# Kernel tuning notes

Hardware: AMD Instinct MI355X
Metric: run time of the kernel (lower is better)

The kernel has to match this reference:

```python
import jax, jax.numpy as jnp
import numpy as np

K = 31   # avg_pool2d kernel_size
PAD = 15 # avg_pool2d padding (count_include_pad=True -> divide by K*K always)


def box_mean(x):
    # x: (N, C, H, W). Zero-padded 31x31 box filter, stride 1, same output size.
    s = jax.lax.reduce_window(
        x, 0.0, jax.lax.add,
        window_dimensions=(1, 1, K, K),
        window_strides=(1, 1, 1, 1),
        padding=((0, 0), (0, 0), (PAD, PAD), (PAD, PAD)))
    return s / (K * K)


def setup_inputs() -> dict:
    key = jax.random.key(0)
    k1, k2 = jax.random.split(key)
    N, C, H, W = 16, 2, 512, 512
    pred = jax.random.normal(k1, (N, C, H, W), dtype=jnp.float32)
    target = jax.random.randint(k2, (N, H, W), 0, C)  # class labels in [0, C)
    return {"pred": pred, "target": target}


def reference(pred, target):
    LOSS_WEIGHT = 1.0
    N, C, H, W = pred.shape
    # _expand_onehot_labels: clamp to [0, C], one-hot C+1, drop last, NHWC->NCHW
    t = jnp.clip(target, 0, C)
    mask = jnp.transpose(jax.nn.one_hot(t, C + 1, dtype=pred.dtype)[..., :C],
                         (0, 3, 1, 2))  # (N, C, H, W), float
    # ignore_index=255 > C so the channel filter keeps all channels (no-op)

    weit = 1.0 + 5.0 * jnp.abs(box_mean(mask) - mask)

    # F.binary_cross_entropy_with_logits(pred, mask, reduce='none'):
    # legacy `reduce='none'` is truthy -> reduction='mean' in torch, so wbce is
    # the GLOBAL mean of elementwise BCE; the subsequent weighted normalization
    # (weit*wbce).sum/weit.sum is then an identity broadcast. Replicated faithfully.
    bce = jnp.maximum(pred, 0.0) - pred * mask + jnp.log1p(jnp.exp(-jnp.abs(pred)))
    wbce = jnp.mean(bce)  # scalar

    p = jax.nn.sigmoid(pred)
    inter = jnp.sum(p * mask * weit, axis=(2, 3))          # (N, C)
    union = jnp.sum((p + mask) * weit, axis=(2, 3))        # (N, C)
    wiou = 1.0 - (inter + 1.0) / (union - inter + 1.0)     # (N, C)

    return LOSS_WEIGHT * jnp.mean(wbce + wiou)
```

## Files before the change

kernel.cpp:

```cpp
#include <hip/hip_runtime.h>
#include <stdint.h>

#define N_IMG 16
#define H_DIM 512
#define W_DIM 512
#define PADR 15
#define BAND 8
#define HALO (BAND + 2 * PADR)
#define WPR 18
#define NBANDS (H_DIM / BAND)
#define WROW (W_DIM / 32)


__global__ __launch_bounds__(512) void bitmap_kernel(const int* __restrict__ target,
                                                     uint32_t* __restrict__ bm) {
    const int tid = threadIdx.x;
    const size_t idx = (size_t)blockIdx.x * 512 + tid;
    const int t = target[idx];
    const unsigned long long bal = __ballot(t == 1);
    if ((tid & 31) == 0)
        bm[idx >> 5] = (tid & 32) ? (uint32_t)(bal >> 32) : (uint32_t)bal;
}

__global__ __launch_bounds__(512, 8) void mega_kernel(const uint32_t* __restrict__ bm,
                                                      const float* __restrict__ pred,
                                                      float* __restrict__ part) {
    __shared__ uint32_t B[HALO][WPR];
    const int tid = threadIdx.x;
    const int band = blockIdx.x;
    const int n = blockIdx.y;
    const int r0 = band * BAND;
    const int col = tid;

    const uint32_t* __restrict__ bmn = bm + (size_t)n * H_DIM * WROW;
    const int hr0 = tid >> 4, wi = tid & 15;
    const int ra = r0 - PADR + hr0;
    uint32_t w0 = 0, w1 = 0;
    if (ra >= 0 && ra < H_DIM) w0 = bmn[ra * WROW + wi];
    const int hr1 = hr0 + 32;
    const int rb = r0 - PADR + hr1;
    if (tid < 96 && rb >= 0 && rb < H_DIM) w1 = bmn[rb * WROW + wi];

    const size_t img = (size_t)n * H_DIM * W_DIM;
    const float* __restrict__ p0 = pred + img * 2 + (size_t)r0 * W_DIM + col;
    const float* __restrict__ p1 = p0 + (size_t)H_DIM * W_DIM;
    float x0[BAND], x1[BAND];
#pragma unroll
    for (int rr = 0; rr < BAND; ++rr) {
        x0[rr] = p0[rr * W_DIM];
        x1[rr] = p1[rr * W_DIM];
    }

    if (tid < 2 * HALO) B[tid >> 1][(tid & 1) ? (WPR - 1) : 0] = 0u;
    B[hr0][1 + wi] = w0;
    if (tid < 96) B[hr1][1 + wi] = w1;
    __syncthreads();

    const int b = col + (32 - PADR);
    const int q = b >> 5, s = b & 31;
    auto wpop = [&](int i) -> uint32_t {
        const uint32_t lo = B[i][q];
        const uint32_t hi = B[i][q + 1];
        const uint32_t val =
            (uint32_t)((((uint64_t)hi << 32) | lo) >> s) & 0x7FFFFFFFu;
        return val;
    };

    uint32_t run = 0, mbits = 0;
#pragma unroll
    for (int i = 0; i < 31; ++i) {
        const uint32_t val = wpop(i);
        run += (uint32_t)__popc(val);
        if (i >= PADR && i < PADR + BAND)
            mbits |= ((val >> PADR) & 1u) << (i - PADR);
    }

    const int cntw = min(col + PADR, W_DIM - 1) - max(col - PADR, 0) + 1;
    const float inv961 = 1.0f / 961.0f;
    float bce = 0.f, in0 = 0.f, in1 = 0.f, un0 = 0.f, un1 = 0.f;

#pragma unroll
    for (int rr = 0; rr < BAND; ++rr) {
        const int r = r0 + rr;
        const int cnth = min(r + PADR, H_DIM - 1) - max(r - PADR, 0) + 1;
        const float cnt = (float)(cnth * cntw);
        const float m1 = (float)((mbits >> rr) & 1u);
        const float m0 = 1.0f - m1;
        const float V = (float)run;
        const float box1 = V * inv961;
        const float box0 = (cnt - V) * inv961;
        const float w1f = 1.0f + 5.0f * fabsf(box1 - m1);
        const float w0f = 1.0f + 5.0f * fabsf(box0 - m0);
        {
            const float x = x0[rr];
            const float t = __expf(-fabsf(x));
            const float inv = 1.0f / (1.0f + t);
            const float p = (x >= 0.f) ? inv : t * inv;
            bce += fmaxf(x, 0.f) - x * m0 + __logf(1.0f + t);
            in0 += p * m0 * w0f;
            un0 += (p + m0) * w0f;
        }
        {
            const float x = x1[rr];
            const float t = __expf(-fabsf(x));
            const float inv = 1.0f / (1.0f + t);
            const float p = (x >= 0.f) ? inv : t * inv;
            bce += fmaxf(x, 0.f) - x * m1 + __logf(1.0f + t);
            in1 += p * m1 * w1f;
            un1 += (p + m1) * w1f;
        }
        if (rr < BAND - 1)
            run += (uint32_t)__popc(wpop(rr + 31)) - (uint32_t)__popc(wpop(rr));
    }

    __shared__ float red[8 * 5];
    const int lane = tid & 63, wv = tid >> 6;
    float v[5] = {bce, in0, in1, un0, un1};
#pragma unroll
    for (int k = 0; k < 5; ++k)
#pragma unroll
        for (int off = 32; off > 0; off >>= 1)
            v[k] += __shfl_down(v[k], off);
    if (lane == 0)
#pragma unroll
        for (int k = 0; k < 5; ++k) red[wv * 5 + k] = v[k];
    __syncthreads();
    if (tid == 0) {
        float s2[5];
#pragma unroll
        for (int k = 0; k < 5; ++k) {
            s2[k] = red[k];
            for (int w2 = 1; w2 < 8; ++w2) s2[k] += red[w2 * 5 + k];
        }
        float* p = part + (size_t)(n * NBANDS + band) * 5;
#pragma unroll
        for (int k = 0; k < 5; ++k) p[k] = s2[k];
    }
}

__global__ __launch_bounds__(256) void finalize_kernel(const float* __restrict__ part,
                                                       float* __restrict__ out) {
    const int tid = threadIdx.x;
    const int n = tid >> 4;
    const int i = tid & 15;
    float bce = 0.f, in0 = 0.f, in1 = 0.f, un0 = 0.f, un1 = 0.f;
#pragma unroll
    for (int j = 0; j < 4; ++j) {
        const float* p = part + (size_t)(n * NBANDS + j * 16 + i) * 5;
        bce += p[0]; in0 += p[1]; in1 += p[2]; un0 += p[3]; un1 += p[4];
    }
#pragma unroll
    for (int off = 8; off > 0; off >>= 1) {
        bce += __shfl_xor(bce, off, 16);
        in0 += __shfl_xor(in0, off, 16);
        in1 += __shfl_xor(in1, off, 16);
        un0 += __shfl_xor(un0, off, 16);
        un1 += __shfl_xor(un1, off, 16);
    }
    __shared__ float fb[16], fw[16];
    if (i == 0) {
        fb[n] = bce;
        fw[n] = (1.0f - (in0 + 1.0f) / (un0 - in0 + 1.0f)) +
                (1.0f - (in1 + 1.0f) / (un1 - in1 + 1.0f));
    }
    __syncthreads();
    if (tid == 0) {
        float sb = 0.f, sw = 0.f;
#pragma unroll
        for (int k = 0; k < 16; ++k) { sb += fb[k]; sw += fw[k]; }
        out[0] = sb / 8388608.0f + sw * (1.0f / 32.0f);
    }
}

extern "C" void kernel_launch(void* const* d_in, const int* in_sizes, int n_in,
                              void* d_out, int out_size, void* d_ws, size_t ws_size,
                              hipStream_t stream) {
    const float* pred = (const float*)d_in[0];
    const int* target = (const int*)d_in[1];
    float* part = (float*)d_ws;
    uint32_t* bm = (uint32_t*)((char*)d_ws + 32768);

    bitmap_kernel<<<N_IMG * H_DIM, 512, 0, stream>>>(target, bm);
    dim3 grid(NBANDS, N_IMG);
    mega_kernel<<<grid, 512, 0, stream>>>(bm, pred, part);
    finalize_kernel<<<1, 256, 0, stream>>>(part, (float*)d_out);
}
```

Baseline: 27.97 us.

## Fuse finalize into main kernel via atomics and vectorize bitmap packing

Drops the separate finalize kernel. Each block atomically adds its partial sums into per-image accumulators, and the last block to finish, found with an atomic counter, computes the final loss. The bitmap kernel now reads 8 labels per thread with int4 loads, packs them into bytes combined across 4 lanes by shuffles, and zeroes the accumulators. This removes one kernel launch and cuts the bitmap kernel's block count, at the cost of float atomics, which make the summation order nondeterministic.

```diff
diff --git a/kernel.cpp b/kernel.cpp
--- a/kernel.cpp
+++ b/kernel.cpp
@@ -10,22 +10,34 @@
 #define WPR 18
 #define NBANDS (H_DIM / BAND)
 #define WROW (W_DIM / 32)
+#define NBLK (NBANDS * N_IMG)
 
 
-__global__ __launch_bounds__(512) void bitmap_kernel(const int* __restrict__ target,
-                                                     uint32_t* __restrict__ bm) {
+__global__ __launch_bounds__(256) void bitmap_kernel(const int4* __restrict__ tg4,
+                                                     uint32_t* __restrict__ bm,
+                                                     float* __restrict__ acc) {
     const int tid = threadIdx.x;
-    const size_t idx = (size_t)blockIdx.x * 512 + tid;
-    const int t = target[idx];
-    const unsigned long long bal = __ballot(t == 1);
-    if ((tid & 31) == 0)
-        bm[idx >> 5] = (tid & 32) ? (uint32_t)(bal >> 32) : (uint32_t)bal;
+    if (blockIdx.x == 0 && tid < 81) acc[tid] = 0.0f;
+    const size_t t = (size_t)blockIdx.x * 256 + tid;
+    const int4 a = tg4[t * 2];
+    const int4 b = tg4[t * 2 + 1];
+    uint32_t by = (uint32_t)(a.x == 1) | ((uint32_t)(a.y == 1) << 1) |
+                  ((uint32_t)(a.z == 1) << 2) | ((uint32_t)(a.w == 1) << 3) |
+                  ((uint32_t)(b.x == 1) << 4) | ((uint32_t)(b.y == 1) << 5) |
+                  ((uint32_t)(b.z == 1) << 6) | ((uint32_t)(b.w == 1) << 7);
+    uint32_t w = by << (8 * (tid & 3));
+    w |= __shfl_xor(w, 1);
+    w |= __shfl_xor(w, 2);
+    if ((tid & 3) == 0) bm[t >> 2] = w;
 }
 
 __global__ __launch_bounds__(512, 8) void mega_kernel(const uint32_t* __restrict__ bm,
                                                       const float* __restrict__ pred,
-                                                      float* __restrict__ part) {
+                                                      float* __restrict__ acc,
+                                                      float* __restrict__ out) {
     __shared__ uint32_t B[HALO][WPR];
+    __shared__ float red[8 * 5];
+    __shared__ int lastFlag;
     const int tid = threadIdx.x;
     const int band = blockIdx.x;
     const int n = blockIdx.y;
@@ -61,9 +73,7 @@
     auto wpop = [&](int i) -> uint32_t {
         const uint32_t lo = B[i][q];
         const uint32_t hi = B[i][q + 1];
-        const uint32_t val =
-            (uint32_t)((((uint64_t)hi << 32) | lo) >> s) & 0x7FFFFFFFu;
-        return val;
+        return (uint32_t)((((uint64_t)hi << 32) | lo) >> s) & 0x7FFFFFFFu;
     };
 
     uint32_t run = 0, mbits = 0;
@@ -113,7 +123,6 @@
             run += (uint32_t)__popc(wpop(rr + 31)) - (uint32_t)__popc(wpop(rr));
     }
 
-    __shared__ float red[8 * 5];
     const int lane = tid & 63, wv = tid >> 6;
     float v[5] = {bce, in0, in1, un0, un1};
 #pragma unroll
@@ -125,6 +134,11 @@
 #pragma unroll
         for (int k = 0; k < 5; ++k) red[wv * 5 + k] = v[k];
     __syncthreads();
+
+    float* aIn = acc;
+    float* aUn = acc + 32;
+    float* aBce = acc + 64;
+    uint32_t* cnt = (uint32_t*)(acc + 80);
     if (tid == 0) {
         float s2[5];
 #pragma unroll
@@ -132,43 +146,37 @@
             s2[k] = red[k];
             for (int w2 = 1; w2 < 8; ++w2) s2[k] += red[w2 * 5 + k];
         }
-        float* p = part + (size_t)(n * NBANDS + band) * 5;
-#pragma unroll
-        for (int k = 0; k < 5; ++k) p[k] = s2[k];
-    }
-}
-
-__global__ __launch_bounds__(256) void finalize_kernel(const float* __restrict__ part,
-                                                       float* __restrict__ out) {
-    const int tid = threadIdx.x;
-    const int n = tid >> 4;
-    const int i = tid & 15;
-    float bce = 0.f, in0 = 0.f, in1 = 0.f, un0 = 0.f, un1 = 0.f;
-#pragma unroll
-    for (int j = 0; j < 4; ++j) {
-        const float* p = part + (size_t)(n * NBANDS + j * 16 + i) * 5;
-        bce += p[0]; in0 += p[1]; in1 += p[2]; un0 += p[3]; un1 += p[4];
-    }
-#pragma unroll
-    for (int off = 8; off > 0; off >>= 1) {
-        bce += __shfl_xor(bce, off, 16);
-        in0 += __shfl_xor(in0, off, 16);
-        in1 += __shfl_xor(in1, off, 16);
-        un0 += __shfl_xor(un0, off, 16);
-        un1 += __shfl_xor(un1, off, 16);
-    }
-    __shared__ float fb[16], fw[16];
-    if (i == 0) {
-        fb[n] = bce;
-        fw[n] = (1.0f - (in0 + 1.0f) / (un0 - in0 + 1.0f)) +
-                (1.0f - (in1 + 1.0f) / (un1 - in1 + 1.0f));
+        atomicAdd(&aBce[n], s2[0]);
+        atomicAdd(&aIn[n * 2 + 0], s2[1]);
+        atomicAdd(&aIn[n * 2 + 1], s2[2]);
+        atomicAdd(&aUn[n * 2 + 0], s2[3]);
+        atomicAdd(&aUn[n * 2 + 1], s2[4]);
+        __threadfence();
+        lastFlag = (atomicAdd(cnt, 1u) == NBLK - 1);
     }
     __syncthreads();
-    if (tid == 0) {
-        float sb = 0.f, sw = 0.f;
+    if (lastFlag) {
+        __threadfence();
+        float sw = 0.f, sb = 0.f;
+        if (tid < 32) {
+            const float vin = __hip_atomic_load(&aIn[tid], __ATOMIC_RELAXED,
+                                                __HIP_MEMORY_SCOPE_AGENT);
+            const float vun = __hip_atomic_load(&aUn[tid], __ATOMIC_RELAXED,
+                                                __HIP_MEMORY_SCOPE_AGENT);
+            sw = 1.0f - (vin + 1.0f) / (vun - vin + 1.0f);
+        }
+        if (tid < 16)
+            sb = __hip_atomic_load(&aBce[tid], __ATOMIC_RELAXED,
+                                   __HIP_MEMORY_SCOPE_AGENT);
+        if (tid < 64) {
 #pragma unroll
-        for (int k = 0; k < 16; ++k) { sb += fb[k]; sw += fw[k]; }
-        out[0] = sb / 8388608.0f + sw * (1.0f / 32.0f);
+            for (int off = 32; off > 0; off >>= 1) {
+                sw += __shfl_down(sw, off);
+                sb += __shfl_down(sb, off);
+            }
+            if (tid == 0)
+                out[0] = sb / 8388608.0f + sw * (1.0f / 32.0f);
+        }
     }
 }
 
@@ -177,11 +185,10 @@
                               hipStream_t stream) {
     const float* pred = (const float*)d_in[0];
     const int* target = (const int*)d_in[1];
-    float* part = (float*)d_ws;
+    float* acc = (float*)d_ws;
     uint32_t* bm = (uint32_t*)((char*)d_ws + 32768);
 
-    bitmap_kernel<<<N_IMG * H_DIM, 512, 0, stream>>>(target, bm);
+    bitmap_kernel<<<2048, 256, 0, stream>>>((const int4*)target, bm, acc);
     dim3 grid(NBANDS, N_IMG);
-    mega_kernel<<<grid, 512, 0, stream>>>(bm, pred, part);
-    finalize_kernel<<<1, 256, 0, stream>>>(part, (float*)d_out);
+    mega_kernel<<<grid, 512, 0, stream>>>(bm, pred, acc, (float*)d_out);
 }
```

Result: slower. 49.96 us (+78.6%).
